# Kernel tuning notes

Measured on AMD Instinct MI355X. Metric: run time of the kernel, lower is better.

Reference implementation:

```python
import jax, jax.numpy as jnp
import numpy as np

N_NODES = 50000
N_EDGES = 1600000
NODE_DIM = 64
EDGE_DIM = 32
HIDDEN = 128
OUT = 64


def setup_inputs() -> dict:
    key = jax.random.key(0)
    k1, k2, k3, k4, k5, k6, k7 = jax.random.split(key, 7)
    edge_index = jax.random.randint(k1, (2, N_EDGES), 0, N_NODES, dtype=jnp.int64 if jax.config.jax_enable_x64 else jnp.int32)
    node_features = jax.random.normal(k2, (N_NODES, NODE_DIM), dtype=jnp.float32)
    edge_features = jax.random.normal(k3, (N_EDGES, EDGE_DIM), dtype=jnp.float32)
    in_dim = EDGE_DIM + 2 * NODE_DIM
    # torch nn.Linear init scale ~ 1/sqrt(fan_in)
    W1 = jax.random.uniform(k4, (HIDDEN, in_dim), jnp.float32, -1.0, 1.0) / np.sqrt(in_dim)
    b1 = jax.random.uniform(k5, (HIDDEN,), jnp.float32, -1.0, 1.0) / np.sqrt(in_dim)
    W2 = jax.random.uniform(k6, (OUT, HIDDEN), jnp.float32, -1.0, 1.0) / np.sqrt(HIDDEN)
    b2 = jax.random.uniform(k7, (OUT,), jnp.float32, -1.0, 1.0) / np.sqrt(HIDDEN)
    return {"edge_index": edge_index, "node_features": node_features,
            "edge_features": edge_features, "W1": W1, "b1": b1, "W2": W2, "b2": b2}


def reference(edge_index, node_features, edge_features, W1, b1, W2, b2):
    src = node_features[edge_index[0]]  # [E, node_dim]
    tgt = node_features[edge_index[1]]  # [E, node_dim]
    x = jnp.concatenate([edge_features, src, tgt], axis=1)  # [E, edge_dim + 2*node_dim]
    h = jax.nn.relu(x @ W1.T + b1)  # [E, hidden]
    return h @ W2.T + b2  # [E, out]
```

## Files before the change

### kernel.cpp

```cpp
#include <hip/hip_runtime.h>

typedef __bf16 bf16x4 __attribute__((ext_vector_type(4)));
typedef __bf16 bf16x8 __attribute__((ext_vector_type(8)));
typedef float  f32x4  __attribute__((ext_vector_type(4)));
typedef unsigned int u32x4 __attribute__((ext_vector_type(4)));

#define XS  168
#define HS2 132

__device__ inline f32x4 mfma16(bf16x8 a, bf16x8 b, f32x4 c) {
  return __builtin_amdgcn_mfma_f32_16x16x32_bf16(a, b, c, 0, 0, 0);
}

struct bf2 { __bf16 h, l; };
__device__ inline bf2 split(float x) {
  bf2 r;
  r.h = (__bf16)x;
  r.l = (__bf16)(x - (float)r.h);
  return r;
}
__device__ inline unsigned int bfbits(__bf16 x) {
  return (unsigned int)__builtin_bit_cast(unsigned short, x);
}

__global__ __launch_bounds__(256, 2) void edge_mlp(
    const int* __restrict__ eidx, const float* __restrict__ nf,
    const float* __restrict__ ef, const float* __restrict__ W1,
    const float* __restrict__ b1, const float* __restrict__ W2,
    const float* __restrict__ b2, float* __restrict__ out, int E)
{
  __shared__ __bf16 sXh[64 * XS];
  __shared__ __bf16 sXl[64 * XS];
  __shared__ unsigned int sH2[64 * HS2];

  const int tid  = threadIdx.x;
  const int lane = tid & 63;
  const int wv   = tid >> 6;
  const int l16  = lane & 15;
  const int q    = lane >> 4;

  bf16x8 w1h[2][5], w1l[2][5];
#pragma unroll
  for (int nt = 0; nt < 2; ++nt) {
    const int j = 32 * wv + 16 * nt + l16;
#pragma unroll
    for (int kc = 0; kc < 5; ++kc) {
      const float* p = W1 + j * 160 + kc * 32 + q * 8;
#pragma unroll
      for (int i = 0; i < 8; ++i) {
        bf2 s = split(p[i]);
        w1h[nt][kc][i] = s.h;
        w1l[nt][kc][i] = s.l;
      }
    }
  }
  bf16x8 w2h[4], w2l[4];
  {
    const int o = 16 * wv + l16;
#pragma unroll
    for (int kc = 0; kc < 4; ++kc) {
      const float* p = W2 + o * 128 + kc * 32 + q * 8;
#pragma unroll
      for (int i = 0; i < 8; ++i) {
        bf2 s = split(p[i]);
        w2h[kc][i] = s.h;
        w2l[kc][i] = s.l;
      }
    }
  }
  const float b1j0 = b1[32 * wv + l16];
  const float b1j1 = b1[32 * wv + 16 + l16];
  const float b2o  = b2[16 * wv + l16];

  const float4* ef4 = (const float4*)ef;
  const float4* nf4 = (const float4*)nf;

  const int eL = tid >> 2;
  const int qq = tid & 3;
  const int ntiles = (E + 63) >> 6;

  float4 g[10];
  auto gather = [&](int tile_) {
    int e = tile_ * 64 + eL;
    if (e >= E) e = E - 1;
    const int s = eidx[e];
    const int t = eidx[E + e];
#pragma unroll
    for (int i = 0; i < 10; ++i) {
      const int fi = qq + 4 * i;
      const float4* p = (i < 2) ? (ef4 + e * 8 + fi)
                      : (i < 6) ? (nf4 + s * 16 + (fi - 8))
                                : (nf4 + t * 16 + (fi - 24));
      g[i] = *p;
    }
  };

  int tile = blockIdx.x;
  if (tile < ntiles) gather(tile);

  for (; tile < ntiles; tile += gridDim.x) {
    const int e0 = tile << 6;

#pragma unroll
    for (int i = 0; i < 10; ++i) {
      const int fi = qq + 4 * i;
      const float4 v = g[i];
      bf16x4 hv, lv;
      { bf2 s0 = split(v.x); hv[0] = s0.h; lv[0] = s0.l; }
      { bf2 s1 = split(v.y); hv[1] = s1.h; lv[1] = s1.l; }
      { bf2 s2 = split(v.z); hv[2] = s2.h; lv[2] = s2.l; }
      { bf2 s3 = split(v.w); hv[3] = s3.h; lv[3] = s3.l; }
      *(bf16x4*)&sXh[eL * XS + fi * 4] = hv;
      *(bf16x4*)&sXl[eL * XS + fi * 4] = lv;
    }
    __syncthreads();

    {
      const int nxt = tile + gridDim.x;
      if (nxt < ntiles) gather(nxt);
    }

    f32x4 acc1[4][2];
#pragma unroll
    for (int mt = 0; mt < 4; ++mt)
#pragma unroll
      for (int nt = 0; nt < 2; ++nt)
        acc1[mt][nt] = (f32x4){0.f, 0.f, 0.f, 0.f};

#pragma unroll
    for (int kc = 0; kc < 5; ++kc) {
#pragma unroll
      for (int mp = 0; mp < 4; mp += 2) {
        bf16x8 ah[2], al[2];
#pragma unroll
        for (int m = 0; m < 2; ++m) {
          ah[m] = *(const bf16x8*)&sXh[(16 * (mp + m) + l16) * XS + kc * 32 + q * 8];
          al[m] = *(const bf16x8*)&sXl[(16 * (mp + m) + l16) * XS + kc * 32 + q * 8];
        }
#pragma unroll
        for (int m = 0; m < 2; ++m)
#pragma unroll
          for (int nt = 0; nt < 2; ++nt)
            acc1[mp + m][nt] = mfma16(ah[m], w1h[nt][kc], acc1[mp + m][nt]);
#pragma unroll
        for (int m = 0; m < 2; ++m)
#pragma unroll
          for (int nt = 0; nt < 2; ++nt)
            acc1[mp + m][nt] = mfma16(ah[m], w1l[nt][kc], acc1[mp + m][nt]);
#pragma unroll
        for (int m = 0; m < 2; ++m)
#pragma unroll
          for (int nt = 0; nt < 2; ++nt)
            acc1[mp + m][nt] = mfma16(al[m], w1h[nt][kc], acc1[mp + m][nt]);
      }
    }

#pragma unroll
    for (int mt = 0; mt < 4; ++mt) {
#pragma unroll
      for (int nt = 0; nt < 2; ++nt) {
        const int col = 32 * wv + 16 * nt + l16;
        const float bb = nt ? b1j1 : b1j0;
#pragma unroll
        for (int r = 0; r < 4; ++r) {
          float h = fmaxf(acc1[mt][nt][r] + bb, 0.f);
          bf2 s = split(h);
          sH2[(16 * mt + 4 * q + r) * HS2 + col] = bfbits(s.h) | (bfbits(s.l) << 16);
        }
      }
    }
    __syncthreads();

    f32x4 acc2[4];
#pragma unroll
    for (int mt = 0; mt < 4; ++mt) acc2[mt] = (f32x4){0.f, 0.f, 0.f, 0.f};

#pragma unroll
    for (int kc = 0; kc < 4; ++kc) {
      bf16x8 ah[4], al[4];
#pragma unroll
      for (int mt = 0; mt < 4; ++mt) {
        const unsigned int* base = &sH2[(16 * mt + l16) * HS2 + kc * 32 + q * 8];
        const u32x4 u0 = *(const u32x4*)base;
        const u32x4 u1 = *(const u32x4*)(base + 4);
        u32x4 hh, ll;
        hh.x = __builtin_amdgcn_perm(u0.y, u0.x, 0x05040100u);
        hh.y = __builtin_amdgcn_perm(u0.w, u0.z, 0x05040100u);
        hh.z = __builtin_amdgcn_perm(u1.y, u1.x, 0x05040100u);
        hh.w = __builtin_amdgcn_perm(u1.w, u1.z, 0x05040100u);
        ll.x = __builtin_amdgcn_perm(u0.y, u0.x, 0x07060302u);
        ll.y = __builtin_amdgcn_perm(u0.w, u0.z, 0x07060302u);
        ll.z = __builtin_amdgcn_perm(u1.y, u1.x, 0x07060302u);
        ll.w = __builtin_amdgcn_perm(u1.w, u1.z, 0x07060302u);
        ah[mt] = __builtin_bit_cast(bf16x8, hh);
        al[mt] = __builtin_bit_cast(bf16x8, ll);
      }
#pragma unroll
      for (int mt = 0; mt < 4; ++mt) acc2[mt] = mfma16(ah[mt], w2h[kc], acc2[mt]);
#pragma unroll
      for (int mt = 0; mt < 4; ++mt) acc2[mt] = mfma16(ah[mt], w2l[kc], acc2[mt]);
#pragma unroll
      for (int mt = 0; mt < 4; ++mt) acc2[mt] = mfma16(al[mt], w2h[kc], acc2[mt]);
    }

#pragma unroll
    for (int mt = 0; mt < 4; ++mt) {
#pragma unroll
      for (int r = 0; r < 4; ++r) {
        const int e = e0 + 16 * mt + 4 * q + r;
        if (e < E) out[e * 64 + 16 * wv + l16] = acc2[mt][r] + b2o;
      }
    }
  }
}

extern "C" void kernel_launch(void* const* d_in, const int* in_sizes, int n_in,
                              void* d_out, int out_size, void* d_ws, size_t ws_size,
                              hipStream_t stream) {
  const int*   eidx = (const int*)d_in[0];
  const float* nf   = (const float*)d_in[1];
  const float* ef   = (const float*)d_in[2];
  const float* W1   = (const float*)d_in[3];
  const float* b1   = (const float*)d_in[4];
  const float* W2   = (const float*)d_in[5];
  const float* b2   = (const float*)d_in[6];
  float* out = (float*)d_out;
  const int E = in_sizes[0] / 2;

  dim3 grid(1024), block(256);
  hipLaunchKernelGGL(edge_mlp, grid, block, 0, stream,
                     eidx, nf, ef, W1, b1, W2, b2, out, E);
}
```

Measured before the change: 736.2 us.

## Swap MFMA operand roles, alias shared buffers, and raise occupancy to three blocks

Swaps the A/B operands of the MFMAs so each lane's accumulator holds four consecutive output features of one edge. This allows vectorized bf16x4 stores into split hi/lo hidden planes and 16-byte float4 output stores, replacing the per-element scattered stores and perm unpacking. The hidden-layer buffer now aliases the input-tile shared memory, cutting LDS use, so launch bounds rise to 3 blocks per CU and the grid to 1536. The cost is an extra __syncthreads per tile to protect the aliased buffer, plus tighter register pressure at the higher occupancy.

```diff
diff --git a/kernel.cpp b/kernel.cpp
--- a/kernel.cpp
+++ b/kernel.cpp
@@ -3,10 +3,11 @@
 typedef __bf16 bf16x4 __attribute__((ext_vector_type(4)));
 typedef __bf16 bf16x8 __attribute__((ext_vector_type(8)));
 typedef float  f32x4  __attribute__((ext_vector_type(4)));
-typedef unsigned int u32x4 __attribute__((ext_vector_type(4)));
-
-#define XS  168
-#define HS2 132
+
+#define XS 168
+#define HS 136
+#define XPLANE (64 * XS * 2)
+#define HPLANE (64 * HS * 2)
 
 __device__ inline f32x4 mfma16(bf16x8 a, bf16x8 b, f32x4 c) {
   return __builtin_amdgcn_mfma_f32_16x16x32_bf16(a, b, c, 0, 0, 0);
@@ -19,19 +20,18 @@
   r.l = (__bf16)(x - (float)r.h);
   return r;
 }
-__device__ inline unsigned int bfbits(__bf16 x) {
-  return (unsigned int)__builtin_bit_cast(unsigned short, x);
-}
-
-__global__ __launch_bounds__(256, 2) void edge_mlp(
+
+__global__ __launch_bounds__(256, 3) void edge_mlp(
     const int* __restrict__ eidx, const float* __restrict__ nf,
     const float* __restrict__ ef, const float* __restrict__ W1,
     const float* __restrict__ b1, const float* __restrict__ W2,
     const float* __restrict__ b2, float* __restrict__ out, int E)
 {
-  __shared__ __bf16 sXh[64 * XS];
-  __shared__ __bf16 sXl[64 * XS];
-  __shared__ unsigned int sH2[64 * HS2];
+  __shared__ __attribute__((aligned(16))) char smem[2 * XPLANE];
+  __bf16* const sXh = (__bf16*)smem;
+  __bf16* const sXl = (__bf16*)(smem + XPLANE);
+  __bf16* const sHh = (__bf16*)smem;
+  __bf16* const sHl = (__bf16*)(smem + HPLANE);
 
   const int tid  = threadIdx.x;
   const int lane = tid & 63;
@@ -41,16 +41,16 @@
 
   bf16x8 w1h[2][5], w1l[2][5];
 #pragma unroll
-  for (int nt = 0; nt < 2; ++nt) {
-    const int j = 32 * wv + 16 * nt + l16;
+  for (int jt = 0; jt < 2; ++jt) {
+    const int j = 32 * wv + 16 * jt + l16;
 #pragma unroll
     for (int kc = 0; kc < 5; ++kc) {
       const float* p = W1 + j * 160 + kc * 32 + q * 8;
 #pragma unroll
       for (int i = 0; i < 8; ++i) {
         bf2 s = split(p[i]);
-        w1h[nt][kc][i] = s.h;
-        w1l[nt][kc][i] = s.l;
+        w1h[jt][kc][i] = s.h;
+        w1l[jt][kc][i] = s.l;
       }
     }
   }
@@ -68,9 +68,13 @@
       }
     }
   }
-  const float b1j0 = b1[32 * wv + l16];
-  const float b1j1 = b1[32 * wv + 16 + l16];
-  const float b2o  = b2[16 * wv + l16];
+  float b1v[2][4], b2v[4];
+#pragma unroll
+  for (int jt = 0; jt < 2; ++jt)
+#pragma unroll
+    for (int r = 0; r < 4; ++r) b1v[jt][r] = b1[32 * wv + 16 * jt + 4 * q + r];
+#pragma unroll
+  for (int r = 0; r < 4; ++r) b2v[r] = b2[16 * wv + 4 * q + r];
 
   const float4* ef4 = (const float4*)ef;
   const float4* nf4 = (const float4*)nf;
@@ -100,6 +104,8 @@
 
   for (; tile < ntiles; tile += gridDim.x) {
     const int e0 = tile << 6;
+
+    __syncthreads();
 
 #pragma unroll
     for (int i = 0; i < 10; ++i) {
@@ -120,95 +126,90 @@
       if (nxt < ntiles) gather(nxt);
     }
 
-    f32x4 acc1[4][2];
-#pragma unroll
-    for (int mt = 0; mt < 4; ++mt)
-#pragma unroll
-      for (int nt = 0; nt < 2; ++nt)
-        acc1[mt][nt] = (f32x4){0.f, 0.f, 0.f, 0.f};
+    f32x4 acc1[2][4];
+#pragma unroll
+    for (int jt = 0; jt < 2; ++jt)
+#pragma unroll
+      for (int et = 0; et < 4; ++et) acc1[jt][et] = (f32x4){0.f, 0.f, 0.f, 0.f};
 
 #pragma unroll
     for (int kc = 0; kc < 5; ++kc) {
 #pragma unroll
-      for (int mp = 0; mp < 4; mp += 2) {
-        bf16x8 ah[2], al[2];
+      for (int ep = 0; ep < 4; ep += 2) {
+        bf16x8 xh[2], xl[2];
 #pragma unroll
         for (int m = 0; m < 2; ++m) {
-          ah[m] = *(const bf16x8*)&sXh[(16 * (mp + m) + l16) * XS + kc * 32 + q * 8];
-          al[m] = *(const bf16x8*)&sXl[(16 * (mp + m) + l16) * XS + kc * 32 + q * 8];
+          const int off = (16 * (ep + m) + l16) * XS + kc * 32 + q * 8;
+          xh[m] = *(const bf16x8*)&sXh[off];
+          xl[m] = *(const bf16x8*)&sXl[off];
         }
 #pragma unroll
         for (int m = 0; m < 2; ++m)
 #pragma unroll
-          for (int nt = 0; nt < 2; ++nt)
-            acc1[mp + m][nt] = mfma16(ah[m], w1h[nt][kc], acc1[mp + m][nt]);
+          for (int jt = 0; jt < 2; ++jt)
+            acc1[jt][ep + m] = mfma16(w1h[jt][kc], xh[m], acc1[jt][ep + m]);
 #pragma unroll
         for (int m = 0; m < 2; ++m)
 #pragma unroll
-          for (int nt = 0; nt < 2; ++nt)
-            acc1[mp + m][nt] = mfma16(ah[m], w1l[nt][kc], acc1[mp + m][nt]);
+          for (int jt = 0; jt < 2; ++jt)
+            acc1[jt][ep + m] = mfma16(w1h[jt][kc], xl[m], acc1[jt][ep + m]);
 #pragma unroll
         for (int m = 0; m < 2; ++m)
 #pragma unroll
-          for (int nt = 0; nt < 2; ++nt)
-            acc1[mp + m][nt] = mfma16(al[m], w1h[nt][kc], acc1[mp + m][nt]);
-      }
-    }
-
-#pragma unroll
-    for (int mt = 0; mt < 4; ++mt) {
-#pragma unroll
-      for (int nt = 0; nt < 2; ++nt) {
-        const int col = 32 * wv + 16 * nt + l16;
-        const float bb = nt ? b1j1 : b1j0;
+          for (int jt = 0; jt < 2; ++jt)
+            acc1[jt][ep + m] = mfma16(w1l[jt][kc], xh[m], acc1[jt][ep + m]);
+      }
+    }
+
+    __syncthreads();
+
+#pragma unroll
+    for (int jt = 0; jt < 2; ++jt) {
+#pragma unroll
+      for (int et = 0; et < 4; ++et) {
+        bf16x4 hh, hl;
 #pragma unroll
         for (int r = 0; r < 4; ++r) {
-          float h = fmaxf(acc1[mt][nt][r] + bb, 0.f);
+          const float h = fmaxf(acc1[jt][et][r] + b1v[jt][r], 0.f);
           bf2 s = split(h);
-          sH2[(16 * mt + 4 * q + r) * HS2 + col] = bfbits(s.h) | (bfbits(s.l) << 16);
+          hh[r] = s.h; hl[r] = s.l;
         }
+        const int base = (16 * et + l16) * HS + 32 * wv + 16 * jt + 4 * q;
+        *(bf16x4*)&sHh[base] = hh;
+        *(bf16x4*)&sHl[base] = hl;
       }
     }
     __syncthreads();
 
     f32x4 acc2[4];
 #pragma unroll
-    for (int mt = 0; mt < 4; ++mt) acc2[mt] = (f32x4){0.f, 0.f, 0.f, 0.f};
+    for (int et = 0; et < 4; ++et) acc2[et] = (f32x4){0.f, 0.f, 0.f, 0.f};
 
 #pragma unroll
     for (int kc = 0; kc < 4; ++kc) {
-      bf16x8 ah[4], al[4];
-#pragma unroll
-      for (int mt = 0; mt < 4; ++mt) {
-        const unsigned int* base = &sH2[(16 * mt + l16) * HS2 + kc * 32 + q * 8];
-        const u32x4 u0 = *(const u32x4*)base;
-        const u32x4 u1 = *(const u32x4*)(base + 4);
-        u32x4 hh, ll;
-        hh.x = __builtin_amdgcn_perm(u0.y, u0.x, 0x05040100u);
-        hh.y = __builtin_amdgcn_perm(u0.w, u0.z, 0x05040100u);
-        hh.z = __builtin_amdgcn_perm(u1.y, u1.x, 0x05040100u);
-        hh.w = __builtin_amdgcn_perm(u1.w, u1.z, 0x05040100u);
-        ll.x = __builtin_amdgcn_perm(u0.y, u0.x, 0x07060302u);
-        ll.y = __builtin_amdgcn_perm(u0.w, u0.z, 0x07060302u);
-        ll.z = __builtin_amdgcn_perm(u1.y, u1.x, 0x07060302u);
-        ll.w = __builtin_amdgcn_perm(u1.w, u1.z, 0x07060302u);
-        ah[mt] = __builtin_bit_cast(bf16x8, hh);
-        al[mt] = __builtin_bit_cast(bf16x8, ll);
-      }
-#pragma unroll
-      for (int mt = 0; mt < 4; ++mt) acc2[mt] = mfma16(ah[mt], w2h[kc], acc2[mt]);
-#pragma unroll
-      for (int mt = 0; mt < 4; ++mt) acc2[mt] = mfma16(ah[mt], w2l[kc], acc2[mt]);
-#pragma unroll
-      for (int mt = 0; mt < 4; ++mt) acc2[mt] = mfma16(al[mt], w2h[kc], acc2[mt]);
-    }
-
-#pragma unroll
-    for (int mt = 0; mt < 4; ++mt) {
-#pragma unroll
-      for (int r = 0; r < 4; ++r) {
-        const int e = e0 + 16 * mt + 4 * q + r;
-        if (e < E) out[e * 64 + 16 * wv + l16] = acc2[mt][r] + b2o;
+      bf16x8 hh[4], hl[4];
+#pragma unroll
+      for (int et = 0; et < 4; ++et) {
+        const int off = (16 * et + l16) * HS + kc * 32 + q * 8;
+        hh[et] = *(const bf16x8*)&sHh[off];
+        hl[et] = *(const bf16x8*)&sHl[off];
+      }
+#pragma unroll
+      for (int et = 0; et < 4; ++et) acc2[et] = mfma16(w2h[kc], hh[et], acc2[et]);
+#pragma unroll
+      for (int et = 0; et < 4; ++et) acc2[et] = mfma16(w2h[kc], hl[et], acc2[et]);
+#pragma unroll
+      for (int et = 0; et < 4; ++et) acc2[et] = mfma16(w2l[kc], hh[et], acc2[et]);
+    }
+
+#pragma unroll
+    for (int et = 0; et < 4; ++et) {
+      const int e = e0 + 16 * et + l16;
+      if (e < E) {
+        f32x4 o;
+#pragma unroll
+        for (int r = 0; r < 4; ++r) o[r] = acc2[et][r] + b2v[r];
+        *(f32x4*)&out[e * 64 + 16 * wv + 4 * q] = o;
       }
     }
   }
@@ -227,7 +228,7 @@
   float* out = (float*)d_out;
   const int E = in_sizes[0] / 2;
 
-  dim3 grid(1024), block(256);
+  dim3 grid(1536), block(256);
   hipLaunchKernelGGL(edge_mlp, grid, block, 0, stream,
                      eidx, nf, ef, W1, b1, W2, b2, out, E);
 }
```

New measurement: 894.2 us. 21.5% more time.
